# Optimization experiments

Measured on AMD Instinct MI355X. Metric: run time of the kernel, lower is better.

Reference implementation:

```python
import jax, jax.numpy as jnp
import numpy as np

TEMPERATURE = 0.05
SINKHORN_ITERS = 10


def setup_inputs() -> dict:
    key = jax.random.key(0)
    ks = jax.random.split(key, 6)
    N, D, E = 4096, 300, 32768
    x = jax.random.normal(ks[0], (N, D), dtype=jnp.float32)
    W1 = jax.random.normal(ks[1], (D, D), dtype=jnp.float32) * 0.05
    b1 = jax.random.normal(ks[2], (D,), dtype=jnp.float32) * 0.01
    W2 = jax.random.normal(ks[3], (D, D), dtype=jnp.float32) * 0.05
    b2 = jax.random.normal(ks[4], (D,), dtype=jnp.float32) * 0.01
    edge_index = jax.random.randint(ks[5], (2, E), 0, N, dtype=jnp.int64)
    return {"x": x, "W1": W1, "b1": b1, "W2": W2, "b2": b2,
            "edge_index": edge_index}


def _sinkhorn(dot):
    # dot: [N, N]; batch dim of 1 in the original collapses away.
    in_size = dot.shape[0]
    out_size = dot.shape[1]
    K = jnp.exp(dot)
    v = jnp.ones((out_size,), dtype=K.dtype)
    a = jnp.asarray(out_size / in_size, dtype=K.dtype)
    u = jnp.ones((in_size,), dtype=K.dtype)
    for _ in range(SINKHORN_ITERS):
        u = a / (K @ v)            # [N]
        v = 1.0 / (u @ K)          # [N]
    return u[:, None] * (K * v[None, :])  # [N, N] coupling


def reference(x, W1, b1, W2, b2, edge_index):
    N = x.shape[0]
    # projector: Linear -> ReLU -> Linear
    out = jax.nn.relu(x @ W1 + b1) @ W2 + b2
    # L2 normalize rows (torch F.normalize with eps=1e-12)
    norm = jnp.maximum(jnp.linalg.norm(out, axis=1, keepdims=True), 1e-12)
    node_features = out / norm
    logits = (node_features @ node_features.T) / TEMPERATURE  # [N, N]
    log_probs = jax.nn.log_softmax(logits, axis=1)
    # Sinkhorn coupling computed under no_grad in the original
    coupling = jax.lax.stop_gradient(_sinkhorn(logits))
    loss = -jnp.mean(jnp.sum(coupling * log_probs, axis=1))
    # dense 2-hop adjacency target
    src, dst = edge_index[0], edge_index[1]
    adj = jnp.zeros((N, N), dtype=jnp.float32).at[src, dst].set(1.0)
    adj = adj + jnp.eye(N, dtype=jnp.float32)
    adj2 = ((adj @ adj) > 0).astype(jnp.float32)
    targets = adj2 / jnp.sum(adj2, axis=0, keepdims=True)
    loss = loss + (-jnp.mean(jnp.sum(targets * log_probs, axis=1)))
    return loss
```

## Files before the change

### kernel.cpp

```cpp
#include <hip/hip_runtime.h>
#include <cstdint>
#include <cstddef>

#define N 4096
#define D 300
#define KP 320
#define INV_T 20.0f
#define SK_ITERS 10
#define NTILE 528

typedef __attribute__((ext_vector_type(8))) short bf16x8;
typedef __attribute__((ext_vector_type(4))) float f32x4;
typedef __attribute__((ext_vector_type(8))) unsigned short ushort8;

__device__ inline void tile_decode(int blk, int& bi, int& bj) {
  int lin = (blk & 7) * 66 + (blk >> 3);
  int a = 0;
  while (lin >= 32 - a) { lin -= 32 - a; ++a; }
  bi = a; bj = a + lin;
}

__global__ void zero_u32(unsigned int* __restrict__ p, int n) {
  int i = blockIdx.x * 256 + threadIdx.x;
  int stride = gridDim.x * 256;
  for (; i < n; i += stride) p[i] = 0u;
}

__global__ __launch_bounds__(320) void mlp_gemm(const float* __restrict__ A,
                                                const float* __restrict__ B,
                                                const float* __restrict__ bias,
                                                float* __restrict__ C, int relu) {
  __shared__ __align__(16) float As[4][304];
  int r0 = blockIdx.x * 4;
  for (int idx = threadIdx.x; idx < 4 * 300; idx += 320) {
    int r = idx / 300, k = idx - r * 300;
    As[r][k] = A[(size_t)(r0 + r) * D + k];
  }
  __syncthreads();
  int c = threadIdx.x;
  if (c < D) {
    float acc[4] = {0, 0, 0, 0};
    for (int k = 0; k < D; k += 4) {
      float b0 = B[(size_t)(k + 0) * D + c];
      float b1 = B[(size_t)(k + 1) * D + c];
      float b2 = B[(size_t)(k + 2) * D + c];
      float b3 = B[(size_t)(k + 3) * D + c];
#pragma unroll
      for (int r = 0; r < 4; ++r) {
        const float4 a4 = *reinterpret_cast<const float4*>(&As[r][k]);
        acc[r] += a4.x * b0 + a4.y * b1 + a4.z * b2 + a4.w * b3;
      }
    }
#pragma unroll
    for (int r = 0; r < 4; ++r) {
      float o = acc[r] + bias[c];
      if (relu) o = fmaxf(o, 0.0f);
      C[(size_t)(r0 + r) * D + c] = o;
    }
  }
}

__device__ inline unsigned short bf16_rne(float v) {
  unsigned int u = __float_as_uint(v);
  unsigned int r = u + 0x7fffu + ((u >> 16) & 1u);
  return (unsigned short)(r >> 16);
}

__global__ __launch_bounds__(64) void normalize_split(const float* __restrict__ in,
                                                      unsigned short* __restrict__ fhi,
                                                      unsigned short* __restrict__ flo) {
  int row = blockIdx.x;
  const float* r = in + (size_t)row * D;
  float ss = 0.0f;
  for (int c = threadIdx.x; c < D; c += 64) {
    float v = r[c];
    ss += v * v;
  }
  for (int o = 32; o > 0; o >>= 1) ss += __shfl_down(ss, o);
  ss = __shfl(ss, 0);
  float inv = 1.0f / fmaxf(sqrtf(ss), 1e-12f);
  for (int c = threadIdx.x; c < KP; c += 64) {
    float v = (c < D) ? r[c] * inv : 0.0f;
    unsigned short h = bf16_rne(v);
    float hf = __uint_as_float((unsigned int)h << 16);
    unsigned short lo = bf16_rne(v - hf);
    fhi[(size_t)row * KP + c] = h;
    flo[(size_t)row * KP + c] = lo;
  }
}

__global__ __launch_bounds__(256) void logits_mfma(const unsigned short* __restrict__ fhi,
                                                   const unsigned short* __restrict__ flo,
                                                   float* __restrict__ logits,
                                                   unsigned short* __restrict__ kexp) {
  __shared__ __align__(16) unsigned short smem[16896];
  int bi, bj;
  tile_decode(blockIdx.x, bi, bj);
  int row0 = bi * 128, col0 = bj * 128;
  int tid = threadIdx.x;
  int w = tid >> 6, l = tid & 63;
  int wr = w >> 1, wc = w & 1;
  f32x4 acc[4][4] = {};

  for (int k0 = 0; k0 < KP; k0 += 32) {
    ushort8 stg[8];
#pragma unroll
    for (int t = 0; t < 8; ++t) {
      int c = t * 256 + tid;
      int b = c >> 9, i = c & 511, row = i >> 2, k16 = i & 3;
      const unsigned short* base = (b & 1) ? flo : fhi;
      int blk = (b < 2) ? row0 : col0;
      stg[t] = *reinterpret_cast<const ushort8*>(
          &base[(size_t)(blk + row) * KP + k0 + k16 * 8]);
    }
    __syncthreads();
#pragma unroll
    for (int t = 0; t < 8; ++t) {
      int c = t * 256 + tid;
      *reinterpret_cast<ushort8*>(&smem[c * 8]) = stg[t];
    }
    __syncthreads();

    bf16x8 ah[4], al[4], bh[4], bl[4];
#pragma unroll
    for (int m = 0; m < 4; ++m) {
      int off = (wr * 64 + m * 16 + (l & 15)) * 32 + (l >> 4) * 8;
      ah[m] = *reinterpret_cast<const bf16x8*>(&smem[0 * 4096 + off]);
      al[m] = *reinterpret_cast<const bf16x8*>(&smem[1 * 4096 + off]);
    }
#pragma unroll
    for (int n = 0; n < 4; ++n) {
      int off = (wc * 64 + n * 16 + (l & 15)) * 32 + (l >> 4) * 8;
      bh[n] = *reinterpret_cast<const bf16x8*>(&smem[2 * 4096 + off]);
      bl[n] = *reinterpret_cast<const bf16x8*>(&smem[3 * 4096 + off]);
    }
#pragma unroll
    for (int m = 0; m < 4; ++m)
#pragma unroll
      for (int n = 0; n < 4; ++n) {
        acc[m][n] = __builtin_amdgcn_mfma_f32_16x16x32_bf16(ah[m], bh[n], acc[m][n], 0, 0, 0);
        acc[m][n] = __builtin_amdgcn_mfma_f32_16x16x32_bf16(ah[m], bl[n], acc[m][n], 0, 0, 0);
        acc[m][n] = __builtin_amdgcn_mfma_f32_16x16x32_bf16(al[m], bh[n], acc[m][n], 0, 0, 0);
      }
  }

  float* sf = reinterpret_cast<float*>(smem);
  int rsub = (l >> 4) * 4, csub = l & 15;
#pragma unroll
  for (int half = 0; half < 2; ++half) {
    __syncthreads();
    if (wr == half) {
#pragma unroll
      for (int m = 0; m < 4; ++m)
#pragma unroll
        for (int n = 0; n < 4; ++n) {
          int lcol = wc * 64 + n * 16 + csub;
#pragma unroll
          for (int j = 0; j < 4; ++j)
            sf[(m * 16 + rsub + j) * 132 + lcol] = acc[m][n][j] * INV_T;
        }
    }
    __syncthreads();
#pragma unroll
    for (int it = 0; it < 8; ++it) {
      int idx = it * 256 + tid;
      int lr = idx >> 5, lc4 = idx & 31;
      float4 val = reinterpret_cast<const float4*>(sf)[lr * 33 + lc4];
      int grow = row0 + half * 64 + lr;
      *reinterpret_cast<float4*>(&logits[(size_t)grow * N + col0 + lc4 * 4]) = val;
      ushort4 kv;
      kv.x = bf16_rne(__expf(val.x));
      kv.y = bf16_rne(__expf(val.y));
      kv.z = bf16_rne(__expf(val.z));
      kv.w = bf16_rne(__expf(val.w));
      *reinterpret_cast<ushort4*>(&kexp[(size_t)grow * N + col0 + lc4 * 4]) = kv;
    }
  }
}

__global__ __launch_bounds__(256) void sk_fused(const unsigned short* __restrict__ kexp,
                                                const float* __restrict__ totprev,
                                                float* __restrict__ totcur,
                                                float* __restrict__ totnext,
                                                float* __restrict__ lse,
                                                int first, int write_lse) {
  __shared__ float red[16][8][17];
  __shared__ float vrow[128], vcol[128];
  int bi, bj;
  tile_decode(blockIdx.x, bi, bj);
  int row0 = bi * 128, col0 = bj * 128;
  int t = threadIdx.x;
  if (t < 8) {
    int zb = blockIdx.x * 8 + t;
    if (zb < N) totnext[zb] = 0.f;
  }
  if (first) {
    if (t < 128) vrow[t] = 1.f;
    else vcol[t - 128] = 1.f;
  } else {
    if (t < 128) {
      float tt = totprev[row0 + t];
      vrow[t] = 1.f / tt;
      if (write_lse && bi == bj) lse[row0 + t] = logf(tt);
    } else {
      vcol[t - 128] = 1.f / totprev[col0 + (t - 128)];
    }
  }
  __syncthreads();
  int ty = t >> 4, tx = t & 15;
  int r0 = ty * 8, c0 = tx * 8;
  float vc[8];
#pragma unroll
  for (int j = 0; j < 8; ++j) vc[j] = vcol[c0 + j];
  float cs[8] = {};
  float rsa[8];
#pragma unroll
  for (int i = 0; i < 8; ++i) {
    const ushort8 kv = *reinterpret_cast<const ushort8*>(
        &kexp[(size_t)(row0 + r0 + i) * N + col0 + c0]);
    float vri = vrow[r0 + i];
    float rs = 0.f;
#pragma unroll
    for (int j = 0; j < 8; ++j) {
      float e = __uint_as_float((unsigned int)(unsigned short)kv[j] << 16);
      rs += e * vc[j];
      cs[j] += e * vri;
    }
    rsa[i] = rs;
  }
#pragma unroll
  for (int i = 0; i < 8; ++i) red[ty][i][tx] = rsa[i];
  __syncthreads();
  if (t < 128) {
    float s = 0.f;
#pragma unroll
    for (int x = 0; x < 16; ++x) s += red[t >> 3][t & 7][x];
    atomicAdd(&totcur[row0 + t], s);
  }
  if (bi != bj) {
    __syncthreads();
#pragma unroll
    for (int j = 0; j < 8; ++j) red[tx][j][ty] = cs[j];
    __syncthreads();
    if (t < 128) {
      float s = 0.f;
#pragma unroll
      for (int y = 0; y < 16; ++y) s += red[t >> 3][t & 7][y];
      atomicAdd(&totcur[col0 + t], s);
    }
  }
}

__global__ void invert2(const float* __restrict__ a, const float* __restrict__ b,
                        float* __restrict__ ua, float* __restrict__ vb) {
  int i = blockIdx.x * 256 + threadIdx.x;
  ua[i] = 1.f / a[i];
  vb[i] = 1.f / b[i];
}

__global__ __launch_bounds__(256) void loss1_tile(const float* __restrict__ logits,
                                                  const float* __restrict__ v,
                                                  float* __restrict__ pr0,
                                                  float* __restrict__ pr1) {
  __shared__ float red[16][8][17];
  int bi, bj;
  tile_decode(blockIdx.x, bi, bj);
  int row0 = bi * 128, col0 = bj * 128;
  int t = threadIdx.x, ty = t >> 4, tx = t & 15;
  int r0 = ty * 8, c0 = tx * 8;
  float vc[8];
  *reinterpret_cast<float4*>(&vc[0]) = *reinterpret_cast<const float4*>(&v[col0 + c0]);
  *reinterpret_cast<float4*>(&vc[4]) = *reinterpret_cast<const float4*>(&v[col0 + c0 + 4]);
  float cs0[8] = {}, cs1[8] = {};
  float rs0a[8], rs1a[8];
#pragma unroll
  for (int i = 0; i < 8; ++i) {
    const float* lp = logits + (size_t)(row0 + r0 + i) * N + col0 + c0;
    float4 q0 = *reinterpret_cast<const float4*>(lp);
    float4 q1 = *reinterpret_cast<const float4*>(lp + 4);
    float ql[8] = {q0.x, q0.y, q0.z, q0.w, q1.x, q1.y, q1.z, q1.w};
    float vri = v[row0 + r0 + i];
    float rs0 = 0.f, rs1 = 0.f;
#pragma unroll
    for (int j = 0; j < 8; ++j) {
      float l = ql[j];
      float e = __expf(l);
      float wv = e * vc[j];
      rs0 += wv; rs1 += wv * l;
      cs0[j] += e * vri; cs1[j] += e * vri * l;
    }
    rs0a[i] = rs0; rs1a[i] = rs1;
  }
  size_t up = ((size_t)bi * 32 + bj) * 128;
  size_t dn = ((size_t)bj * 32 + bi) * 128;
#pragma unroll
  for (int i = 0; i < 8; ++i) red[ty][i][tx] = rs0a[i];
  __syncthreads();
  if (t < 128) {
    float s = 0.f;
#pragma unroll
    for (int x = 0; x < 16; ++x) s += red[t >> 3][t & 7][x];
    pr0[up + t] = s;
  }
  __syncthreads();
#pragma unroll
  for (int i = 0; i < 8; ++i) red[ty][i][tx] = rs1a[i];
  __syncthreads();
  if (t < 128) {
    float s = 0.f;
#pragma unroll
    for (int x = 0; x < 16; ++x) s += red[t >> 3][t & 7][x];
    pr1[up + t] = s;
  }
  if (bi != bj) {
    __syncthreads();
#pragma unroll
    for (int j = 0; j < 8; ++j) red[tx][j][ty] = cs0[j];
    __syncthreads();
    if (t < 128) {
      float s = 0.f;
#pragma unroll
      for (int y = 0; y < 16; ++y) s += red[t >> 3][t & 7][y];
      pr0[dn + t] = s;
    }
    __syncthreads();
#pragma unroll
    for (int j = 0; j < 8; ++j) red[tx][j][ty] = cs1[j];
    __syncthreads();
    if (t < 128) {
      float s = 0.f;
#pragma unroll
      for (int y = 0; y < 16; ++y) s += red[t >> 3][t & 7][y];
      pr1[dn + t] = s;
    }
  }
}

__global__ __launch_bounds__(256) void loss1_reduce(const float* __restrict__ pr0,
                                                    const float* __restrict__ pr1,
                                                    const float* __restrict__ u,
                                                    const float* __restrict__ lse,
                                                    double* __restrict__ term1) {
  int i = blockIdx.x * 256 + threadIdx.x;
  int a = i >> 7, ri = i & 127;
  double s0 = 0.0, s1 = 0.0;
#pragma unroll
  for (int s = 0; s < 32; ++s) {
    s0 += (double)pr0[((size_t)a * 32 + s) * 128 + ri];
    s1 += (double)pr1[((size_t)a * 32 + s) * 128 + ri];
  }
  term1[i] = (double)u[i] * (s1 - (double)lse[i] * s0);
}

__global__ void build_adj(const int* __restrict__ ei, int E,
                          unsigned int* __restrict__ adjmask, int* __restrict__ deg) {
  int t = blockIdx.x * 256 + threadIdx.x;
  if (t < E) {
    int s = ei[t] & (N - 1), d = ei[E + t] & (N - 1);
    atomicOr(&adjmask[(size_t)s * 128 + (d >> 5)], 1u << (d & 31));
    atomicAdd(&deg[s], 1);
  }
  if (t < N) atomicOr(&adjmask[(size_t)t * 128 + (t >> 5)], 1u << (t & 31));
}

__global__ __launch_bounds__(1024) void scan_deg(const int* __restrict__ deg,
                                                 int* __restrict__ offs,
                                                 int* __restrict__ cursor) {
  __shared__ int part[1024];
  int tid = threadIdx.x;
  int base = tid * 4;
  int l0 = deg[base + 0], l1 = deg[base + 1], l2 = deg[base + 2], l3 = deg[base + 3];
  part[tid] = l0 + l1 + l2 + l3;
  __syncthreads();
  for (int d = 1; d < 1024; d <<= 1) {
    int v = (tid >= d) ? part[tid - d] : 0;
    __syncthreads();
    part[tid] += v;
    __syncthreads();
  }
  int run = (tid > 0) ? part[tid - 1] : 0;
  offs[base + 0] = run; cursor[base + 0] = run; run += l0;
  offs[base + 1] = run; cursor[base + 1] = run; run += l1;
  offs[base + 2] = run; cursor[base + 2] = run; run += l2;
  offs[base + 3] = run; cursor[base + 3] = run;
}

__global__ void scatter_edges(const int* __restrict__ ei, int E,
                              int* __restrict__ cursor, int* __restrict__ neigh) {
  int t = blockIdx.x * 256 + threadIdx.x;
  if (t < E) {
    int s = ei[t] & (N - 1), d = ei[E + t] & (N - 1);
    int slot = atomicAdd(&cursor[s], 1);
    neigh[slot] = d;
  }
}

__global__ __launch_bounds__(128) void adj2_kernel(const unsigned int* __restrict__ adjmask,
                                                   const int* __restrict__ offs,
                                                   const int* __restrict__ deg,
                                                   const int* __restrict__ neigh,
                                                   unsigned int* __restrict__ adj2,
                                                   int* __restrict__ colcount) {
  int i = blockIdx.x, w = threadIdx.x;
  unsigned int acc = adjmask[(size_t)i * 128 + w];
  int o = offs[i], dg = deg[i];
  for (int n = 0; n < dg; ++n) {
    int k = neigh[o + n];
    acc |= adjmask[(size_t)k * 128 + w];
  }
  adj2[(size_t)i * 128 + w] = acc;
  unsigned int m = acc;
  while (m) {
    int b = __ffs(m) - 1;
    m &= m - 1;
    atomicAdd(&colcount[w * 32 + b], 1);
  }
}

__global__ __launch_bounds__(128) void loss2_kernel(const unsigned int* __restrict__ adj2,
                                                    const int* __restrict__ colcount,
                                                    const float* __restrict__ logits,
                                                    const float* __restrict__ lse,
                                                    double* __restrict__ term2) {
  __shared__ float sb[2], sb2[2];
  int i = blockIdx.x, w = threadIdx.x;
  unsigned int m = adj2[(size_t)i * 128 + w];
  float s = 0.0f, sc = 0.0f;
  while (m) {
    int b = __ffs(m) - 1;
    m &= m - 1;
    int j = w * 32 + b;
    float lij = (j < i) ? logits[(size_t)j * N + i] : logits[(size_t)i * N + j];
    float ic = 1.0f / (float)colcount[j];
    s += ic * lij;
    sc += ic;
  }
  for (int o = 32; o > 0; o >>= 1) {
    s += __shfl_down(s, o);
    sc += __shfl_down(sc, o);
  }
  int lane = w & 63, wid = w >> 6;
  if (lane == 0) { sb[wid] = s; sb2[wid] = sc; }
  __syncthreads();
  if (w == 0)
    term2[i] = (double)(sb[0] + sb[1]) - (double)lse[i] * (double)(sb2[0] + sb2[1]);
}

__global__ __launch_bounds__(256) void final_reduce(const double* __restrict__ term1,
                                                    const double* __restrict__ term2,
                                                    float* __restrict__ out) {
  __shared__ double sb[4];
  double s = 0.0;
  for (int i = threadIdx.x; i < N; i += 256) s += term1[i] + term2[i];
  for (int o = 32; o > 0; o >>= 1) s += __shfl_down(s, o);
  int lane = threadIdx.x & 63, wid = threadIdx.x >> 6;
  if (lane == 0) sb[wid] = s;
  __syncthreads();
  if (threadIdx.x == 0) out[0] = (float)(-(sb[0] + sb[1] + sb[2] + sb[3]) / (double)N);
}

extern "C" void kernel_launch(void* const* d_in, const int* in_sizes, int n_in,
                              void* d_out, int out_size, void* d_ws, size_t ws_size,
                              hipStream_t stream) {
  const float* x  = (const float*)d_in[0];
  const float* W1 = (const float*)d_in[1];
  const float* b1 = (const float*)d_in[2];
  const float* W2 = (const float*)d_in[3];
  const float* b2 = (const float*)d_in[4];
  const int* ei = (const int*)d_in[5];
  int E = in_sizes[5] / 2;
  float* outp = (float*)d_out;

  char* w = (char*)d_ws;
  float* logits = (float*)w;  w += (size_t)N * N * 4;
  unsigned short* kexp = (unsigned short*)w; w += (size_t)N * N * 2;
  float* h      = (float*)w;  w += (size_t)N * D * 4;
  float* o2     = (float*)w;  w += (size_t)N * D * 4;
  unsigned short* fhi = (unsigned short*)w; w += (size_t)N * KP * 2;
  unsigned short* flo = (unsigned short*)w; w += (size_t)N * KP * 2;
  float* vecA   = (float*)w;  w += 16384;
  float* vecB   = (float*)w;  w += 16384;
  float* lse    = (float*)w;  w += 16384;
  double* term1 = (double*)w; w += 32768;
  double* term2 = (double*)w; w += 32768;
  float* pr0    = (float*)w;  w += 32 * 32 * 128 * 4;
  float* pr1    = (float*)w;  w += 32 * 32 * 128 * 4;
  float* sb0 = (float*)w;     w += 16384;
  float* sb1 = (float*)w;     w += 16384;
  float* sb2 = (float*)w;     w += 16384;
  unsigned int* adjmask = (unsigned int*)w; w += (size_t)N * 128 * 4;
  int* colcount = (int*)w;    w += 16384;
  int* deg      = (int*)w;    w += 16384;
  int zcount = 3 * N + N * 128 + 4096 + 4096;
  unsigned int* adj2 = (unsigned int*)w; w += (size_t)N * 128 * 4;
  int* offs   = (int*)w;      w += 16384;
  int* cursor = (int*)w;      w += 16384;
  int* neigh  = (int*)w;      w += (size_t)E * 4;

  zero_u32<<<512, 256, 0, stream>>>((unsigned int*)sb0, zcount);

  mlp_gemm<<<N / 4, 320, 0, stream>>>(x, W1, b1, h, 1);
  mlp_gemm<<<N / 4, 320, 0, stream>>>(h, W2, b2, o2, 0);
  normalize_split<<<N, 64, 0, stream>>>(o2, fhi, flo);
  logits_mfma<<<NTILE, 256, 0, stream>>>(fhi, flo, logits, kexp);

  int gmax = (E > N ? E : N);
  build_adj<<<(gmax + 255) / 256, 256, 0, stream>>>(ei, E, adjmask, deg);
  scan_deg<<<1, 1024, 0, stream>>>(deg, offs, cursor);
  scatter_edges<<<(E + 255) / 256, 256, 0, stream>>>(ei, E, cursor, neigh);

  float* bufs[3] = {sb0, sb1, sb2};
  for (int p = 0; p < 2 * SK_ITERS; ++p) {
    sk_fused<<<NTILE, 256, 0, stream>>>(kexp,
        p == 0 ? sb0 : bufs[(p - 1) % 3],
        bufs[p % 3], bufs[(p + 1) % 3], lse,
        p == 0 ? 1 : 0, p == 1 ? 1 : 0);
  }
  invert2<<<N / 256, 256, 0, stream>>>(sb0, sb1, vecA, vecB);

  loss1_tile<<<NTILE, 256, 0, stream>>>(logits, vecB, pr0, pr1);
  loss1_reduce<<<N / 256, 256, 0, stream>>>(pr0, pr1, vecA, lse, term1);

  adj2_kernel<<<N, 128, 0, stream>>>(adjmask, offs, deg, neigh, adj2, colcount);
  loss2_kernel<<<N, 128, 0, stream>>>(adj2, colcount, logits, lse, term2);

  final_reduce<<<1, 256, 0, stream>>>(term1, term2, outp);
}
```

Measured before the change: 322.5 us.

## Store full symmetric exp matrix and replace tiled Sinkhorn with row-dot kernel

The logits kernel now also writes the transposed exp tile for off-diagonal blocks, so the bf16 K matrix is stored in full rather than as the upper triangle. Sinkhorn steps become a simple row matrix-vector kernel with no atomics, no zeroing of accumulators and no separate invert kernel. Each step now reads the full matrix instead of half of it, trading extra memory traffic for coalesced, atomic-free reductions. The logits kernel also gains the cost of strided transposed stores.

```diff
diff --git a/kernel.cpp b/kernel.cpp
--- a/kernel.cpp
+++ b/kernel.cpp
@@ -12,6 +12,10 @@
 typedef __attribute__((ext_vector_type(8))) short bf16x8;
 typedef __attribute__((ext_vector_type(4))) float f32x4;
 typedef __attribute__((ext_vector_type(8))) unsigned short ushort8;
+
+__device__ inline float bf2f(unsigned short u) {
+  return __uint_as_float((unsigned int)u << 16);
+}
 
 __device__ inline void tile_decode(int blk, int& bi, int& bj) {
   int lin = (blk & 7) * 66 + (blk >> 3);
@@ -175,87 +179,68 @@
       kv.w = bf16_rne(__expf(val.w));
       *reinterpret_cast<ushort4*>(&kexp[(size_t)grow * N + col0 + lc4 * 4]) = kv;
     }
-  }
-}
-
-__global__ __launch_bounds__(256) void sk_fused(const unsigned short* __restrict__ kexp,
-                                                const float* __restrict__ totprev,
-                                                float* __restrict__ totcur,
-                                                float* __restrict__ totnext,
-                                                float* __restrict__ lse,
-                                                int first, int write_lse) {
-  __shared__ float red[16][8][17];
-  __shared__ float vrow[128], vcol[128];
-  int bi, bj;
-  tile_decode(blockIdx.x, bi, bj);
-  int row0 = bi * 128, col0 = bj * 128;
+    if (bi != bj) {
+#pragma unroll
+      for (int it = 0; it < 8; ++it) {
+        int idx = it * 256 + tid;
+        int c = idx >> 4, r4 = idx & 15;
+        ushort4 kv;
+        kv.x = bf16_rne(__expf(sf[(r4 * 4 + 0) * 132 + c]));
+        kv.y = bf16_rne(__expf(sf[(r4 * 4 + 1) * 132 + c]));
+        kv.z = bf16_rne(__expf(sf[(r4 * 4 + 2) * 132 + c]));
+        kv.w = bf16_rne(__expf(sf[(r4 * 4 + 3) * 132 + c]));
+        *reinterpret_cast<ushort4*>(
+            &kexp[(size_t)(col0 + c) * N + row0 + half * 64 + r4 * 4]) = kv;
+      }
+    }
+  }
+}
+
+__global__ __launch_bounds__(256) void sk_row(const unsigned short* __restrict__ kexp,
+                                              const float* __restrict__ vin,
+                                              float* __restrict__ vout,
+                                              float* __restrict__ lse,
+                                              int first, int store_lse) {
+  __shared__ float red[4][4];
+  int r0 = blockIdx.x * 4;
   int t = threadIdx.x;
-  if (t < 8) {
-    int zb = blockIdx.x * 8 + t;
-    if (zb < N) totnext[zb] = 0.f;
-  }
+  int c0 = t * 16;
+  float vv[16];
   if (first) {
-    if (t < 128) vrow[t] = 1.f;
-    else vcol[t - 128] = 1.f;
+#pragma unroll
+    for (int j = 0; j < 16; ++j) vv[j] = 1.f;
   } else {
-    if (t < 128) {
-      float tt = totprev[row0 + t];
-      vrow[t] = 1.f / tt;
-      if (write_lse && bi == bj) lse[row0 + t] = logf(tt);
-    } else {
-      vcol[t - 128] = 1.f / totprev[col0 + (t - 128)];
-    }
-  }
-  __syncthreads();
-  int ty = t >> 4, tx = t & 15;
-  int r0 = ty * 8, c0 = tx * 8;
-  float vc[8];
-#pragma unroll
-  for (int j = 0; j < 8; ++j) vc[j] = vcol[c0 + j];
-  float cs[8] = {};
-  float rsa[8];
-#pragma unroll
-  for (int i = 0; i < 8; ++i) {
-    const ushort8 kv = *reinterpret_cast<const ushort8*>(
-        &kexp[(size_t)(row0 + r0 + i) * N + col0 + c0]);
-    float vri = vrow[r0 + i];
-    float rs = 0.f;
-#pragma unroll
-    for (int j = 0; j < 8; ++j) {
-      float e = __uint_as_float((unsigned int)(unsigned short)kv[j] << 16);
-      rs += e * vc[j];
-      cs[j] += e * vri;
-    }
-    rsa[i] = rs;
-  }
-#pragma unroll
-  for (int i = 0; i < 8; ++i) red[ty][i][tx] = rsa[i];
-  __syncthreads();
-  if (t < 128) {
+#pragma unroll
+    for (int j = 0; j < 4; ++j)
+      *reinterpret_cast<float4*>(&vv[j * 4]) =
+          *reinterpret_cast<const float4*>(&vin[c0 + j * 4]);
+  }
+  float tot[4];
+#pragma unroll
+  for (int r = 0; r < 4; ++r) {
+    const ushort8 k0 = *reinterpret_cast<const ushort8*>(&kexp[(size_t)(r0 + r) * N + c0]);
+    const ushort8 k1 = *reinterpret_cast<const ushort8*>(&kexp[(size_t)(r0 + r) * N + c0 + 8]);
     float s = 0.f;
 #pragma unroll
-    for (int x = 0; x < 16; ++x) s += red[t >> 3][t & 7][x];
-    atomicAdd(&totcur[row0 + t], s);
-  }
-  if (bi != bj) {
-    __syncthreads();
-#pragma unroll
-    for (int j = 0; j < 8; ++j) red[tx][j][ty] = cs[j];
-    __syncthreads();
-    if (t < 128) {
-      float s = 0.f;
-#pragma unroll
-      for (int y = 0; y < 16; ++y) s += red[t >> 3][t & 7][y];
-      atomicAdd(&totcur[col0 + t], s);
-    }
-  }
-}
-
-__global__ void invert2(const float* __restrict__ a, const float* __restrict__ b,
-                        float* __restrict__ ua, float* __restrict__ vb) {
-  int i = blockIdx.x * 256 + threadIdx.x;
-  ua[i] = 1.f / a[i];
-  vb[i] = 1.f / b[i];
+    for (int j = 0; j < 8; ++j) s += bf2f((unsigned short)k0[j]) * vv[j];
+#pragma unroll
+    for (int j = 0; j < 8; ++j) s += bf2f((unsigned short)k1[j]) * vv[8 + j];
+    tot[r] = s;
+  }
+#pragma unroll
+  for (int o = 32; o > 0; o >>= 1)
+#pragma unroll
+    for (int r = 0; r < 4; ++r) tot[r] += __shfl_down(tot[r], o);
+  int lane = t & 63, w = t >> 6;
+  if (lane == 0) {
+    red[w][0] = tot[0]; red[w][1] = tot[1]; red[w][2] = tot[2]; red[w][3] = tot[3];
+  }
+  __syncthreads();
+  if (t < 4) {
+    float s = red[0][t] + red[1][t] + red[2][t] + red[3][t];
+    vout[r0 + t] = 1.f / s;
+    if (store_lse) lse[r0 + t] = logf(s);
+  }
 }
 
 __global__ __launch_bounds__(256) void loss1_tile(const float* __restrict__ logits,
@@ -485,19 +470,16 @@
   double* term2 = (double*)w; w += 32768;
   float* pr0    = (float*)w;  w += 32 * 32 * 128 * 4;
   float* pr1    = (float*)w;  w += 32 * 32 * 128 * 4;
-  float* sb0 = (float*)w;     w += 16384;
-  float* sb1 = (float*)w;     w += 16384;
-  float* sb2 = (float*)w;     w += 16384;
   unsigned int* adjmask = (unsigned int*)w; w += (size_t)N * 128 * 4;
   int* colcount = (int*)w;    w += 16384;
   int* deg      = (int*)w;    w += 16384;
-  int zcount = 3 * N + N * 128 + 4096 + 4096;
+  int zcount = N * 128 + 4096 + 4096;
   unsigned int* adj2 = (unsigned int*)w; w += (size_t)N * 128 * 4;
   int* offs   = (int*)w;      w += 16384;
   int* cursor = (int*)w;      w += 16384;
   int* neigh  = (int*)w;      w += (size_t)E * 4;
 
-  zero_u32<<<512, 256, 0, stream>>>((unsigned int*)sb0, zcount);
+  zero_u32<<<512, 256, 0, stream>>>(adjmask, zcount);
 
   mlp_gemm<<<N / 4, 320, 0, stream>>>(x, W1, b1, h, 1);
   mlp_gemm<<<N / 4, 320, 0, stream>>>(h, W2, b2, o2, 0);
@@ -509,14 +491,12 @@
   scan_deg<<<1, 1024, 0, stream>>>(deg, offs, cursor);
   scatter_edges<<<(E + 255) / 256, 256, 0, stream>>>(ei, E, cursor, neigh);
 
-  float* bufs[3] = {sb0, sb1, sb2};
+  float* vecs[2] = {vecA, vecB};
   for (int p = 0; p < 2 * SK_ITERS; ++p) {
-    sk_fused<<<NTILE, 256, 0, stream>>>(kexp,
-        p == 0 ? sb0 : bufs[(p - 1) % 3],
-        bufs[p % 3], bufs[(p + 1) % 3], lse,
-        p == 0 ? 1 : 0, p == 1 ? 1 : 0);
-  }
-  invert2<<<N / 256, 256, 0, stream>>>(sb0, sb1, vecA, vecB);
+    sk_row<<<N / 4, 256, 0, stream>>>(kexp,
+        p == 0 ? vecB : vecs[(p + 1) & 1], vecs[p & 1], lse,
+        p == 0 ? 1 : 0, p == 0 ? 1 : 0);
+  }
 
   loss1_tile<<<NTILE, 256, 0, stream>>>(logits, vecB, pr0, pr1);
   loss1_reduce<<<N / 256, 256, 0, stream>>>(pr0, pr1, vecA, lse, term1);
```

After: 323.1 us. Within noise of the previous version (+0.2%).
